# Kernel tuning notes

Hardware: AMD Instinct MI355X
Metric: run time of the kernel (lower is better)

Reference implementation:

```python
import jax, jax.numpy as jnp
import numpy as np

B, S, D, M = 4, 4096, 2048, 512

def _xavier(k, shape):
    return jax.random.normal(k, shape, jnp.float32) * np.float32(np.sqrt(2.0 / (shape[0] + shape[1])))

def setup_inputs() -> dict:
    key = jax.random.key(0)
    ks = jax.random.split(key, 6)
    return dict(
        x=jax.random.normal(ks[0], (B, S, D), jnp.float32),
        memory_state=jnp.zeros((B, M), jnp.float32),
        Wk=_xavier(ks[1], (M, D)), bk=jnp.zeros((M,), jnp.float32),
        Wv=_xavier(ks[2], (M, D)), bv=jnp.zeros((M,), jnp.float32),
        Wg=_xavier(ks[3], (D, D + M)), bg=jnp.zeros((D,), jnp.float32),
        time_decay=jax.random.normal(ks[4], (M,), jnp.float32) * 0.01,
        time_first=jax.random.normal(ks[5], (M,), jnp.float32) * 0.01,
    )

def reference(x, memory_state, Wk, bk, Wv, bv, Wg, bg, time_decay, time_first):
    # decay in (0.1, 1.0) per channel
    td = jax.nn.sigmoid(time_decay) * 0.9 + 0.1          # (M,)
    tf = jax.nn.sigmoid(time_first)                      # (M,)
    # k is computed but never used in the source forward; kept for FLOP parity
    k = jnp.einsum('bsd,md->bsm', x, Wk) + bk
    v = jnp.einsum('bsd,md->bsm', x, Wv) + bv            # (B,S,M)
    # sum_{j<=i} td^(i-j) * v_j  ==  linear recurrence s_i = td*s_{i-1} + v_i
    def step(s, v_t):
        s = td * s + v_t
        return s, s
    _, wv = jax.lax.scan(step, jnp.zeros((x.shape[0], td.shape[0]), x.dtype),
                         jnp.swapaxes(v, 0, 1))          # (S,B,M)
    wv = jnp.swapaxes(wv, 0, 1) + memory_state[:, None, :] * tf  # (B,S,M)
    next_memory_state = wv[:, -1]                        # taken before dropout (eval: identity)
    combined = jnp.concatenate([x, wv], axis=-1)         # (B,S,D+M)
    out = x + jnp.einsum('bse,de->bsd', combined, Wg) + bg
    return out, next_memory_state
```

## Files before the change

### kernel.cpp

```cpp
#include <hip/hip_runtime.h>
#include <hip/hip_bf16.h>
#include <stdint.h>

#define B_ 4
#define S_ 4096
#define D_ 2048
#define M_ 512
#define E_ (D_ + M_)
#define BS_ (B_ * S_)
#define CH_ 32
#define CL_ 128

typedef __attribute__((ext_vector_type(8))) short short8;
typedef __attribute__((ext_vector_type(4))) short short4e;
typedef __attribute__((ext_vector_type(4))) float float4e;

__device__ __forceinline__ unsigned short f2bf(float f) {
    unsigned int u = __float_as_uint(f);
    u = (u + 0x7fffu + ((u >> 16) & 1u)) >> 16;
    return (unsigned short)u;
}
__device__ __forceinline__ float bf2f(unsigned short h) {
    return __uint_as_float(((unsigned int)h) << 16);
}
__device__ __forceinline__ float sigmoidf(float x) {
    return 1.0f / (1.0f + expf(-x));
}

__device__ __forceinline__ void load_lds16(const unsigned short* g, unsigned short* l) {
    __builtin_amdgcn_global_load_lds(
        (const __attribute__((address_space(1))) unsigned int*)g,
        (__attribute__((address_space(3))) unsigned int*)l,
        16, 0, 0);
}

__global__ void conv_x_kernel(const float* __restrict__ x, unsigned short* __restrict__ comb) {
    int i = blockIdx.x * blockDim.x + threadIdx.x;
    const int n4 = BS_ * D_ / 4;
    const int stride = gridDim.x * blockDim.x;
    for (; i < n4; i += stride) {
        int flat = i << 2;
        int row = flat >> 11;
        int col = flat & (D_ - 1);
        float4 xv = ((const float4*)x)[i];
        short4e o = { (short)f2bf(xv.x), (short)f2bf(xv.y),
                      (short)f2bf(xv.z), (short)f2bf(xv.w) };
        *(short4e*)(comb + (size_t)row * E_ + col) = o;
    }
}

__global__ void conv_w_kernel(const float* __restrict__ Wv, unsigned short* __restrict__ Wvb,
                              const float* __restrict__ Wg, unsigned short* __restrict__ Wgb) {
    const int nv4 = M_ * D_ / 4;
    const int ng4 = D_ * E_ / 4;
    int i = blockIdx.x * blockDim.x + threadIdx.x;
    const int stride = gridDim.x * blockDim.x;
    for (; i < nv4 + ng4; i += stride) {
        const float* in;
        unsigned short* out;
        int j;
        if (i < nv4) { in = Wv; out = Wvb; j = i; }
        else         { in = Wg; out = Wgb; j = i - nv4; }
        float4 xv = ((const float4*)in)[j];
        short4e o = { (short)f2bf(xv.x), (short)f2bf(xv.y),
                      (short)f2bf(xv.z), (short)f2bf(xv.w) };
        ((short4e*)out)[j] = o;
    }
}

template<int BM, int BN, bool ADDX, bool OUT_BF16>
__global__ __launch_bounds__(256) void gemm_bt(
    const unsigned short* __restrict__ A, int lda,
    const unsigned short* __restrict__ Bm, int ldb,
    void* __restrict__ Cv, int ldc,
    const float* __restrict__ bias,
    const unsigned short* __restrict__ resid, int resid_ld,
    int K)
{
    constexpr int MI = BM / 32;
    constexpr int NJ = BN / 32;
    constexpr int NGA = BM / 32;
    constexpr int NGB = BN / 32;

    __shared__ unsigned short As[BM * 64];
    __shared__ unsigned short Bs[BN * 64];

    const int tid  = threadIdx.x;
    const int lane = tid & 63;
    const int wave = __builtin_amdgcn_readfirstlane(tid >> 6);
    const int bm0  = blockIdx.x * BM;
    const int bn0  = blockIdx.y * BN;
    const int wm   = wave & 1;
    const int wn   = wave >> 1;
    const int lm   = lane & 15;
    const int quad = lane >> 4;

    const unsigned short* ag[NGA];
    unsigned short* al[NGA];
#pragma unroll
    for (int i = 0; i < NGA; ++i) {
        int g = i * 256 + tid;
        int r = g >> 3, c = g & 7;
        int cg = c ^ (r & 7);
        ag[i] = A + (size_t)(bm0 + r) * lda + cg * 8;
        al[i] = As + (i * 256 + wave * 64) * 8;
    }
    const unsigned short* bgp[NGB];
    unsigned short* bl[NGB];
#pragma unroll
    for (int i = 0; i < NGB; ++i) {
        int g = i * 256 + tid;
        int r = g >> 3, c = g & 7;
        int cg = c ^ (r & 7);
        bgp[i] = Bm + (size_t)(bn0 + r) * ldb + cg * 8;
        bl[i] = Bs + (i * 256 + wave * 64) * 8;
    }

    float4e acc[MI][NJ];
    const float4e zero = {0.f, 0.f, 0.f, 0.f};
#pragma unroll
    for (int i = 0; i < MI; ++i)
#pragma unroll
        for (int j = 0; j < NJ; ++j) acc[i][j] = zero;

    for (int k0 = 0; k0 < K; k0 += 64) {
#pragma unroll
        for (int i = 0; i < NGA; ++i) load_lds16(ag[i] + k0, al[i]);
#pragma unroll
        for (int i = 0; i < NGB; ++i) load_lds16(bgp[i] + k0, bl[i]);
        __syncthreads();
#pragma unroll
        for (int kk = 0; kk < 2; ++kk) {
            short8 af[MI], bf[NJ];
#pragma unroll
            for (int i = 0; i < MI; ++i) {
                int ra = wm * (BM / 2) + i * 16 + lm;
                af[i] = *(const short8*)(As + ra * 64 + (((kk * 4 + quad) ^ (ra & 7)) * 8));
            }
#pragma unroll
            for (int j = 0; j < NJ; ++j) {
                int rb = wn * (BN / 2) + j * 16 + lm;
                bf[j] = *(const short8*)(Bs + rb * 64 + (((kk * 4 + quad) ^ (rb & 7)) * 8));
            }
#pragma unroll
            for (int i = 0; i < MI; ++i)
#pragma unroll
                for (int j = 0; j < NJ; ++j)
                    acc[i][j] = __builtin_amdgcn_mfma_f32_16x16x32_bf16(af[i], bf[j], acc[i][j], 0, 0, 0);
        }
        __syncthreads();
    }

#pragma unroll
    for (int i = 0; i < MI; ++i) {
#pragma unroll
        for (int j = 0; j < NJ; ++j) {
            int row = bm0 + wm * (BM / 2) + i * 16 + quad * 4;
            int col = bn0 + wn * (BN / 2) + j * 16 + lm;
            float bb = bias[col];
#pragma unroll
            for (int r = 0; r < 4; ++r) {
                size_t idx = (size_t)(row + r) * ldc + col;
                float val = acc[i][j][r] + bb;
                if (ADDX) val += bf2f(resid[(size_t)(row + r) * resid_ld + col]);
                if (OUT_BF16) ((unsigned short*)Cv)[idx] = f2bf(val);
                else          ((float*)Cv)[idx] = val;
            }
        }
    }
}

template<bool ADDX, bool OUT_BF16, int MT>
__global__ __launch_bounds__(512, 2) void gemm_bt8(
    const unsigned short* __restrict__ A, int lda,
    const unsigned short* __restrict__ Bm, int ldb,
    void* __restrict__ Cv, int ldc,
    const float* __restrict__ bias,
    const unsigned short* __restrict__ resid, int resid_ld,
    int K)
{
    __shared__ unsigned short As[4][256 * 32];
    __shared__ unsigned short Bs[4][256 * 32];

    const int tid  = threadIdx.x;
    const int lane = tid & 63;
    const int wave = __builtin_amdgcn_readfirstlane(tid >> 6);
    const int wm   = wave >> 2;
    const int wn   = wave & 3;
    const int lm   = lane & 15;
    const int quad = lane >> 4;

    constexpr int RPX = MT / 8;
    const int bid = blockIdx.x;
    const int xcd = bid & 7;
    const int w   = bid >> 3;
    const int row = xcd * RPX + (w % RPX);
    const int col = w / RPX;
    const int bm0 = row * 256;
    const int bn0 = col * 256;

    const unsigned short* agp[2];
    const unsigned short* bgp[2];
    int soffl[2];
#pragma unroll
    for (int s = 0; s < 2; ++s) {
        int g = s * 512 + tid;
        int r = g >> 2, c = g & 3;
        int cg = c ^ ((r >> 1) & 3);
        agp[s] = A  + (size_t)(bm0 + r) * lda + cg * 8;
        bgp[s] = Bm + (size_t)(bn0 + r) * ldb + cg * 8;
        soffl[s] = s * 4096 + wave * 512;
    }

    float4e acc[8][4];
    const float4e zero = {0.f, 0.f, 0.f, 0.f};
#pragma unroll
    for (int i = 0; i < 8; ++i)
#pragma unroll
        for (int j = 0; j < 4; ++j) acc[i][j] = zero;

    const int NT = K >> 5;

#pragma unroll
    for (int s = 0; s < 2; ++s) load_lds16(agp[s], &As[0][soffl[s]]);
#pragma unroll
    for (int s = 0; s < 2; ++s) load_lds16(bgp[s], &Bs[0][soffl[s]]);
#pragma unroll
    for (int s = 0; s < 2; ++s) load_lds16(agp[s] + 32, &As[1][soffl[s]]);
#pragma unroll
    for (int s = 0; s < 2; ++s) load_lds16(bgp[s] + 32, &Bs[1][soffl[s]]);
#pragma unroll
    for (int s = 0; s < 2; ++s) load_lds16(agp[s] + 64, &As[2][soffl[s]]);
#pragma unroll
    for (int s = 0; s < 2; ++s) load_lds16(bgp[s] + 64, &Bs[2][soffl[s]]);
    asm volatile("s_waitcnt vmcnt(8)");
    __builtin_amdgcn_sched_barrier(0);
    __builtin_amdgcn_s_barrier();
    __builtin_amdgcn_sched_barrier(0);

    const int aoff = (wm * 128 + lm) * 32 + ((quad ^ ((lm >> 1) & 3)) << 3);
    const int boff = (wn * 64  + lm) * 32 + ((quad ^ ((lm >> 1) & 3)) << 3);

    for (int t = 0; t < NT; ++t) {
        const int buf = t & 3;
        const unsigned short* Ab = As[buf];
        const unsigned short* Bb = Bs[buf];
        int tp = t + 3; if (tp > NT - 1) tp = NT - 1;
        const int kpre = tp << 5;
        const int pbuf = (t + 3) & 3;

        short8 af[4], bf[4];
#pragma unroll
        for (int i = 0; i < 4; ++i) af[i] = *(const short8*)(Ab + aoff + i * 512);
#pragma unroll
        for (int j = 0; j < 4; ++j) bf[j] = *(const short8*)(Bb + boff + j * 512);
#pragma unroll
        for (int s = 0; s < 2; ++s) load_lds16(agp[s] + kpre, &As[pbuf][soffl[s]]);
        __builtin_amdgcn_s_barrier();
        asm volatile("s_waitcnt lgkmcnt(0)");
        __builtin_amdgcn_sched_barrier(0);
        __builtin_amdgcn_s_setprio(1);
#pragma unroll
        for (int i = 0; i < 4; ++i)
#pragma unroll
            for (int j = 0; j < 4; ++j)
                acc[i][j] = __builtin_amdgcn_mfma_f32_16x16x32_bf16(af[i], bf[j], acc[i][j], 0, 0, 0);
        __builtin_amdgcn_s_setprio(0);
        __builtin_amdgcn_s_barrier();

        short8 ah[4];
#pragma unroll
        for (int i = 0; i < 4; ++i) ah[i] = *(const short8*)(Ab + aoff + (i + 4) * 512);
#pragma unroll
        for (int s = 0; s < 2; ++s) load_lds16(bgp[s] + kpre, &Bs[pbuf][soffl[s]]);
        __builtin_amdgcn_s_barrier();
        asm volatile("s_waitcnt lgkmcnt(0)");
        __builtin_amdgcn_sched_barrier(0);
        __builtin_amdgcn_s_setprio(1);
#pragma unroll
        for (int i = 0; i < 4; ++i)
#pragma unroll
            for (int j = 0; j < 4; ++j)
                acc[i + 4][j] = __builtin_amdgcn_mfma_f32_16x16x32_bf16(ah[i], bf[j], acc[i + 4][j], 0, 0, 0);
        __builtin_amdgcn_s_setprio(0);
        asm volatile("s_waitcnt vmcnt(8)");
        __builtin_amdgcn_sched_barrier(0);
        __builtin_amdgcn_s_barrier();
        __builtin_amdgcn_sched_barrier(0);
    }

#pragma unroll
    for (int i = 0; i < 8; ++i) {
#pragma unroll
        for (int j = 0; j < 4; ++j) {
            int crow = bm0 + wm * 128 + i * 16 + quad * 4;
            int ccol = bn0 + wn * 64  + j * 16 + lm;
            float bb = bias[ccol];
#pragma unroll
            for (int r = 0; r < 4; ++r) {
                size_t idx = (size_t)(crow + r) * ldc + ccol;
                float val = acc[i][j][r] + bb;
                if (ADDX) val += bf2f(resid[(size_t)(crow + r) * resid_ld + ccol]);
                if (OUT_BF16) ((unsigned short*)Cv)[idx] = f2bf(val);
                else          ((float*)Cv)[idx] = val;
            }
        }
    }
}

__global__ void scan_p1(const unsigned short* __restrict__ v, const float* __restrict__ tdp,
                        float* __restrict__ Ebuf) {
    int tid = blockIdx.x * blockDim.x + threadIdx.x;
    int m = tid & (M_ - 1);
    int c = (tid >> 9) & (CH_ - 1);
    int b = tid >> 14;
    float td = 0.9f * sigmoidf(tdp[m]) + 0.1f;
    const unsigned short* vp = v + (size_t)(b * S_ + c * CL_) * M_ + m;
    float s = 0.f;
#pragma unroll 4
    for (int t = 0; t < CL_; ++t) s = td * s + bf2f(vp[(size_t)t * M_]);
    Ebuf[(b * CH_ + c) * M_ + m] = s;
}

__global__ void scan_p3(const unsigned short* __restrict__ v, const float* __restrict__ tdp,
                        const float* __restrict__ tfp, const float* __restrict__ ms,
                        const float* __restrict__ Ebuf, unsigned short* __restrict__ comb,
                        float* __restrict__ out_state) {
    int tid = blockIdx.x * blockDim.x + threadIdx.x;
    int m = tid & (M_ - 1);
    int c = (tid >> 9) & (CH_ - 1);
    int b = tid >> 14;
    float td  = 0.9f * sigmoidf(tdp[m]) + 0.1f;
    float a = td;
#pragma unroll
    for (int i = 0; i < 7; ++i) a *= a;
    float s = 0.f;
    for (int cp = 0; cp < c; ++cp)
        s = a * s + Ebuf[(b * CH_ + cp) * M_ + m];
    float add = ms[b * M_ + m] * sigmoidf(tfp[m]);
    const unsigned short* vp = v + (size_t)(b * S_ + c * CL_) * M_ + m;
    unsigned short* cp_ = comb + (size_t)(b * S_ + c * CL_) * E_ + D_ + m;
    float w = 0.f;
#pragma unroll 4
    for (int t = 0; t < CL_; ++t) {
        s = td * s + bf2f(vp[(size_t)t * M_]);
        w = s + add;
        cp_[(size_t)t * E_] = f2bf(w);
    }
    if (c == CH_ - 1) out_state[b * M_ + m] = w;
}

extern "C" void kernel_launch(void* const* d_in, const int* in_sizes, int n_in,
                              void* d_out, int out_size, void* d_ws, size_t ws_size,
                              hipStream_t stream) {
    const float* x    = (const float*)d_in[0];
    const float* ms   = (const float*)d_in[1];
    const float* Wv   = (const float*)d_in[4];
    const float* bv   = (const float*)d_in[5];
    const float* Wg   = (const float*)d_in[6];
    const float* bg   = (const float*)d_in[7];
    const float* tdec = (const float*)d_in[8];
    const float* tfir = (const float*)d_in[9];

    float* out       = (float*)d_out;
    float* out_state = out + (size_t)BS_ * D_;

    char* ws = (char*)d_ws;
    size_t off = 0;
    unsigned short* comb = (unsigned short*)(ws + off); off += (size_t)BS_ * E_ * 2;
    unsigned short* vbuf = (unsigned short*)(ws + off); off += (size_t)BS_ * M_ * 2;
    unsigned short* Wvb  = (unsigned short*)(ws + off); off += (size_t)M_ * D_ * 2;
    unsigned short* Wgb  = (unsigned short*)(ws + off); off += (size_t)D_ * E_ * 2;
    float*          Ebuf = (float*)(ws + off);          off += (size_t)B_ * CH_ * M_ * 4;

    conv_x_kernel<<<4096, 256, 0, stream>>>(x, comb);
    conv_w_kernel<<<1536, 256, 0, stream>>>(Wv, Wvb, Wg, Wgb);

    gemm_bt<64, 256, false, true><<<dim3(BS_ / 64, M_ / 256), 256, 0, stream>>>(
        comb, E_, Wvb, D_, vbuf, M_, bv, nullptr, 0, D_);

    scan_p1<<<(B_ * CH_ * M_) / 256, 256, 0, stream>>>(vbuf, tdec, Ebuf);
    scan_p3<<<(B_ * CH_ * M_) / 256, 256, 0, stream>>>(vbuf, tdec, tfir, ms, Ebuf, comb, out_state);

    gemm_bt8<true, false, BS_ / 256><<<(BS_ / 256) * (D_ / 256), 512, 0, stream>>>(
        comb, E_, Wgb, E_, out, D_, bg, comb, E_, E_);
}
```

Measured before the change: 525.6 us.

## Restructure bf16 GEMM main loop into double-buffered 64-wide K steps

Replaces the 4-stage, 32-wide K ring of LDS buffers in the gemm_bt8 kernel with two double-buffered 64-wide K stages, each split into two 32-wide halves. Each half loads all eight A fragments once and sweeps the B column fragments in pairs. Prefetch depth drops from three tiles ahead to one 64-wide tile ahead, with vmcnt waits adjusted to match. This cuts loop-iteration and barrier overhead per unit of K and changes register pressure and the interleaving of loads with MFMAs, but it gives less latency hiding for global loads.

```diff
diff --git a/kernel.cpp b/kernel.cpp
--- a/kernel.cpp
+++ b/kernel.cpp
@@ -179,8 +179,8 @@
     const unsigned short* __restrict__ resid, int resid_ld,
     int K)
 {
-    __shared__ unsigned short As[4][256 * 32];
-    __shared__ unsigned short Bs[4][256 * 32];
+    __shared__ unsigned short As[2][2][256 * 32];
+    __shared__ unsigned short Bs[2][2][256 * 32];
 
     const int tid  = threadIdx.x;
     const int lane = tid & 63;
@@ -199,17 +199,17 @@
     const int bm0 = row * 256;
     const int bn0 = col * 256;
 
-    const unsigned short* agp[2];
-    const unsigned short* bgp[2];
-    int soffl[2];
-#pragma unroll
-    for (int s = 0; s < 2; ++s) {
-        int g = s * 512 + tid;
+    const unsigned short* aG[2];
+    const unsigned short* bG[2];
+    int ldsOff[2];
+#pragma unroll
+    for (int l = 0; l < 2; ++l) {
+        int g = l * 512 + tid;
         int r = g >> 2, c = g & 3;
         int cg = c ^ ((r >> 1) & 3);
-        agp[s] = A  + (size_t)(bm0 + r) * lda + cg * 8;
-        bgp[s] = Bm + (size_t)(bn0 + r) * ldb + cg * 8;
-        soffl[s] = s * 4096 + wave * 512;
+        aG[l] = A  + (size_t)(bm0 + r) * lda + cg * 8;
+        bG[l] = Bm + (size_t)(bn0 + r) * ldb + cg * 8;
+        ldsOff[l] = (l * 512 + wave * 64) * 8;
     }
 
     float4e acc[8][4];
@@ -219,74 +219,110 @@
 #pragma unroll
         for (int j = 0; j < 4; ++j) acc[i][j] = zero;
 
-    const int NT = K >> 5;
-
-#pragma unroll
-    for (int s = 0; s < 2; ++s) load_lds16(agp[s], &As[0][soffl[s]]);
-#pragma unroll
-    for (int s = 0; s < 2; ++s) load_lds16(bgp[s], &Bs[0][soffl[s]]);
-#pragma unroll
-    for (int s = 0; s < 2; ++s) load_lds16(agp[s] + 32, &As[1][soffl[s]]);
-#pragma unroll
-    for (int s = 0; s < 2; ++s) load_lds16(bgp[s] + 32, &Bs[1][soffl[s]]);
-#pragma unroll
-    for (int s = 0; s < 2; ++s) load_lds16(agp[s] + 64, &As[2][soffl[s]]);
-#pragma unroll
-    for (int s = 0; s < 2; ++s) load_lds16(bgp[s] + 64, &Bs[2][soffl[s]]);
-    asm volatile("s_waitcnt vmcnt(8)");
+    const int NT = K >> 6;
+
+#pragma unroll
+    for (int l = 0; l < 2; ++l) load_lds16(aG[l],      &As[0][0][ldsOff[l]]);
+#pragma unroll
+    for (int l = 0; l < 2; ++l) load_lds16(bG[l],      &Bs[0][0][ldsOff[l]]);
+#pragma unroll
+    for (int l = 0; l < 2; ++l) load_lds16(aG[l] + 32, &As[0][1][ldsOff[l]]);
+#pragma unroll
+    for (int l = 0; l < 2; ++l) load_lds16(bG[l] + 32, &Bs[0][1][ldsOff[l]]);
+    asm volatile("s_waitcnt vmcnt(4)");
     __builtin_amdgcn_sched_barrier(0);
     __builtin_amdgcn_s_barrier();
     __builtin_amdgcn_sched_barrier(0);
 
-    const int aoff = (wm * 128 + lm) * 32 + ((quad ^ ((lm >> 1) & 3)) << 3);
-    const int boff = (wn * 64  + lm) * 32 + ((quad ^ ((lm >> 1) & 3)) << 3);
-
+    const int swz8 = (quad ^ ((lm >> 1) & 3)) << 3;
+    const int aoff = (wm * 128 + lm) * 32 + swz8;
+    const int boff = (wn * 64  + lm) * 32 + swz8;
+
+    int cur = 0;
     for (int t = 0; t < NT; ++t) {
-        const int buf = t & 3;
-        const unsigned short* Ab = As[buf];
-        const unsigned short* Bb = Bs[buf];
-        int tp = t + 3; if (tp > NT - 1) tp = NT - 1;
-        const int kpre = tp << 5;
-        const int pbuf = (t + 3) & 3;
-
-        short8 af[4], bf[4];
-#pragma unroll
-        for (int i = 0; i < 4; ++i) af[i] = *(const short8*)(Ab + aoff + i * 512);
-#pragma unroll
-        for (int j = 0; j < 4; ++j) bf[j] = *(const short8*)(Bb + boff + j * 512);
-#pragma unroll
-        for (int s = 0; s < 2; ++s) load_lds16(agp[s] + kpre, &As[pbuf][soffl[s]]);
+        const int nxt = cur ^ 1;
+        int tp = t + 1; if (tp > NT - 1) tp = NT - 1;
+        const int kp = tp << 6;
+        const unsigned short* A0 = &As[cur][0][0];
+        const unsigned short* A1 = &As[cur][1][0];
+        const unsigned short* B0 = &Bs[cur][0][0];
+        const unsigned short* B1 = &Bs[cur][1][0];
+
+        short8 af[8], bf0, bf1, bf2, bf3;
+
+#pragma unroll
+        for (int i = 0; i < 8; ++i) af[i] = *(const short8*)(A0 + aoff + i * 512);
+        bf0 = *(const short8*)(B0 + boff);
+        bf1 = *(const short8*)(B0 + boff + 512);
+#pragma unroll
+        for (int l = 0; l < 2; ++l) load_lds16(aG[l] + kp, &As[nxt][0][ldsOff[l]]);
         __builtin_amdgcn_s_barrier();
         asm volatile("s_waitcnt lgkmcnt(0)");
         __builtin_amdgcn_sched_barrier(0);
         __builtin_amdgcn_s_setprio(1);
 #pragma unroll
-        for (int i = 0; i < 4; ++i)
-#pragma unroll
-            for (int j = 0; j < 4; ++j)
-                acc[i][j] = __builtin_amdgcn_mfma_f32_16x16x32_bf16(af[i], bf[j], acc[i][j], 0, 0, 0);
+        for (int i = 0; i < 8; ++i) {
+            acc[i][0] = __builtin_amdgcn_mfma_f32_16x16x32_bf16(af[i], bf0, acc[i][0], 0, 0, 0);
+            acc[i][1] = __builtin_amdgcn_mfma_f32_16x16x32_bf16(af[i], bf1, acc[i][1], 0, 0, 0);
+        }
         __builtin_amdgcn_s_setprio(0);
         __builtin_amdgcn_s_barrier();
 
-        short8 ah[4];
-#pragma unroll
-        for (int i = 0; i < 4; ++i) ah[i] = *(const short8*)(Ab + aoff + (i + 4) * 512);
-#pragma unroll
-        for (int s = 0; s < 2; ++s) load_lds16(bgp[s] + kpre, &Bs[pbuf][soffl[s]]);
+        bf2 = *(const short8*)(B0 + boff + 1024);
+        bf3 = *(const short8*)(B0 + boff + 1536);
+#pragma unroll
+        for (int l = 0; l < 2; ++l) load_lds16(bG[l] + kp, &Bs[nxt][0][ldsOff[l]]);
         __builtin_amdgcn_s_barrier();
         asm volatile("s_waitcnt lgkmcnt(0)");
         __builtin_amdgcn_sched_barrier(0);
         __builtin_amdgcn_s_setprio(1);
 #pragma unroll
-        for (int i = 0; i < 4; ++i)
-#pragma unroll
-            for (int j = 0; j < 4; ++j)
-                acc[i + 4][j] = __builtin_amdgcn_mfma_f32_16x16x32_bf16(ah[i], bf[j], acc[i + 4][j], 0, 0, 0);
+        for (int i = 0; i < 8; ++i) {
+            acc[i][2] = __builtin_amdgcn_mfma_f32_16x16x32_bf16(af[i], bf2, acc[i][2], 0, 0, 0);
+            acc[i][3] = __builtin_amdgcn_mfma_f32_16x16x32_bf16(af[i], bf3, acc[i][3], 0, 0, 0);
+        }
         __builtin_amdgcn_s_setprio(0);
-        asm volatile("s_waitcnt vmcnt(8)");
-        __builtin_amdgcn_sched_barrier(0);
-        __builtin_amdgcn_s_barrier();
-        __builtin_amdgcn_sched_barrier(0);
+        asm volatile("s_waitcnt vmcnt(4)");
+        __builtin_amdgcn_sched_barrier(0);
+        __builtin_amdgcn_s_barrier();
+
+#pragma unroll
+        for (int i = 0; i < 8; ++i) af[i] = *(const short8*)(A1 + aoff + i * 512);
+        bf0 = *(const short8*)(B1 + boff);
+        bf1 = *(const short8*)(B1 + boff + 512);
+#pragma unroll
+        for (int l = 0; l < 2; ++l) load_lds16(aG[l] + kp + 32, &As[nxt][1][ldsOff[l]]);
+        __builtin_amdgcn_s_barrier();
+        asm volatile("s_waitcnt lgkmcnt(0)");
+        __builtin_amdgcn_sched_barrier(0);
+        __builtin_amdgcn_s_setprio(1);
+#pragma unroll
+        for (int i = 0; i < 8; ++i) {
+            acc[i][0] = __builtin_amdgcn_mfma_f32_16x16x32_bf16(af[i], bf0, acc[i][0], 0, 0, 0);
+            acc[i][1] = __builtin_amdgcn_mfma_f32_16x16x32_bf16(af[i], bf1, acc[i][1], 0, 0, 0);
+        }
+        __builtin_amdgcn_s_setprio(0);
+        __builtin_amdgcn_s_barrier();
+
+        bf2 = *(const short8*)(B1 + boff + 1024);
+        bf3 = *(const short8*)(B1 + boff + 1536);
+#pragma unroll
+        for (int l = 0; l < 2; ++l) load_lds16(bG[l] + kp + 32, &Bs[nxt][1][ldsOff[l]]);
+        __builtin_amdgcn_s_barrier();
+        asm volatile("s_waitcnt lgkmcnt(0)");
+        __builtin_amdgcn_sched_barrier(0);
+        __builtin_amdgcn_s_setprio(1);
+#pragma unroll
+        for (int i = 0; i < 8; ++i) {
+            acc[i][2] = __builtin_amdgcn_mfma_f32_16x16x32_bf16(af[i], bf2, acc[i][2], 0, 0, 0);
+            acc[i][3] = __builtin_amdgcn_mfma_f32_16x16x32_bf16(af[i], bf3, acc[i][3], 0, 0, 0);
+        }
+        __builtin_amdgcn_s_setprio(0);
+        asm volatile("s_waitcnt vmcnt(4)");
+        __builtin_amdgcn_sched_barrier(0);
+        __builtin_amdgcn_s_barrier();
+
+        cur = nxt;
     }
 
 #pragma unroll
```

Result: faster. 494.9 us (-5.8%).
